# Kernel optimization log

Hardware: AMD Instinct MI355X
Metric: run time of the kernel (lower is better)

## Reference

```python
import jax, jax.numpy as jnp
import numpy as np

N = 256          # Preisach mesh resolution (n)
T = 2000         # number of applied-field time steps
H_MIN, H_MAX = 0.0, 1.0


def setup_inputs() -> dict:
    key = jax.random.key(0)
    k1, = jax.random.split(key, 1)
    h = jax.random.uniform(k1, (T,), dtype=jnp.float32)  # applied field history
    vec_shape = N * (N + 1) // 2  # = n^2/2 + n/2 = 32896
    raw_density = jnp.ones((vec_shape,), dtype=jnp.float32)  # _raw_hyst_density_vector
    offset = jnp.zeros((1,), dtype=jnp.float32)
    scale = jnp.ones((1,), dtype=jnp.float32)
    return {"h": h, "raw_density": raw_density, "offset": offset, "scale": scale}


def reference(h, raw_density, offset, scale):
    dtype = h.dtype
    # asymmetric mesh on [0,1]: alpha (yy) varies along rows, beta (xx) along cols
    x = jnp.linspace(0.0, 1.0, N, dtype=dtype)
    yy = jnp.broadcast_to(x[:, None], (N, N))  # alpha thresholds
    xx = jnp.broadcast_to(x[None, :], (N, N))  # beta thresholds
    tril_mask = jnp.tril(jnp.ones((N, N), dtype=dtype))

    h_norm = (h - H_MIN) / (H_MAX - H_MIN)  # normalize_h
    hs = jnp.concatenate([jnp.full((1,), H_MIN, dtype=dtype), h_norm])

    # initial state: all hysterions off, then tril (matches states[0] of original)
    init_state = -tril_mask

    def step(state, hp):
        h_prev, h_cur = hp
        swept_up = jnp.where(yy >= h_cur, state, 1.0)    # increasing field
        swept_down = jnp.where(xx <= h_cur, state, -1.0) # decreasing field
        new = jnp.where(h_cur > h_prev, swept_up,
                        jnp.where(h_cur < h_prev, swept_down, state))
        new = new * tril_mask  # torch.tril
        return new, new

    # scan over (hs[i-1], hs[i]) pairs -> states[1:] of the original, shape (T, N, N)
    _, states = jax.lax.scan(step, init_state, (hs[:-1], hs[1:]))

    # density: softplus then vector_to_tril (row-major lower-triangular fill)
    dens_vec = jax.nn.softplus(raw_density)
    ii, jj = jnp.tril_indices(N)
    dens = jnp.zeros((N, N), dtype=dtype).at[ii, jj].set(dens_vec)

    tri_size = N * (N + 1) / 2.0  # get_upper_trainagle_size(n)
    b = jnp.einsum('tjk,jk->t', states, dens) / tri_size
    return b * scale[0] + offset[0]
```

## Files before the change

### kernel.cpp

```cpp
#include <hip/hip_runtime.h>
#include <math.h>


#define CL 32
#define GSZ (518 * 64)
#define AS1 __attribute__((address_space(1)))
#define AS3 __attribute__((address_space(3)))

__device__ __forceinline__ int make_code(const float* __restrict__ h, int t, int T) {
    const float delta = 1.0f / 255.0f;
    int code = 256;
    if (t < T) {
        const float hc = h[t];
        const float hp = (t == 0) ? 0.0f : h[t - 1];
        if (hc > hp) {
            int i2 = (int)(hc * 255.0f);
            if (i2 > 255) i2 = 255;
            while (i2 < 255 && (float)(i2 + 1) * delta < hc) ++i2;
            while (i2 >= 0 && (float)i2 * delta >= hc) --i2;
            code = ((i2 + 1) << 16) | 256;
        } else if (hc < hp) {
            int kk = (int)(hc * 255.0f);
            if (kk > 255) kk = 255;
            while (kk < 255 && (float)(kk + 1) * delta <= hc) ++kk;
            while (kk > 0 && (float)kk * delta > hc) --kk;
            code = kk;
        }
    }
    return code;
}

__global__ __launch_bounds__(256)
void k1_compose_gbuild(const float* __restrict__ h, const float* __restrict__ raw,
                       int* __restrict__ codes, int2* __restrict__ lohi,
                       int2* __restrict__ glohi, float* __restrict__ Gg,
                       int T, int NCH, int NB1) {
    const int b = blockIdx.x;
    const int tid = threadIdx.x;
    const int w = tid >> 6, l = tid & 63;
    if (b < NB1) {
        __shared__ int2 slh[4][256];
        const int q = b * 4 + w;
        int mycode = 256;
        if (q < NCH && l < CL) {
            mycode = make_code(h, q * CL + l, T);
            codes[q * CL + l] = mycode;
        }
        int lo[4] = {-1, -1, -1, -1}, hi[4] = {256, 256, 256, 256};
        #pragma unroll
        for (int s = 0; s < CL; ++s) {
            const int cd = __shfl(mycode, s);
            const int k = cd & 0xFFFF, u = cd >> 16;
            #pragma unroll
            for (int j = 0; j < 4; ++j) {
                const int r = j * 64 + l;
                const int rr = (r < u) ? r : -1;
                lo[j] = max(min(lo[j], k), rr);
                hi[j] = max(min(hi[j], k), rr);
            }
        }
        #pragma unroll
        for (int j = 0; j < 4; ++j) {
            slh[w][j * 64 + l] = make_int2(lo[j], hi[j]);
            if (q < NCH) lohi[q * 256 + j * 64 + l] = make_int2(lo[j], hi[j]);
        }
        __syncthreads();
        int glo = -1, ghi = 256;
        #pragma unroll
        for (int w2 = 0; w2 < 4; ++w2) {
            const int2 lh = slh[w2][tid];
            glo = max(min(glo, lh.y), lh.x);
            ghi = max(min(ghi, lh.y), lh.x);
        }
        glohi[b * 256 + tid] = make_int2(glo, ghi);
    } else {
        const int r = (b - NB1) * 4 + w;
        const int tri = r * (r + 1) / 2;
        int lcol, idx0;
        if (r < 64)       { lcol = r;       idx0 = 0; }
        else if (r < 128) { lcol = r - 64;  idx0 = 259; }
        else if (r < 192) { lcol = 191 - r; idx0 = 325 + lcol; }
        else              { lcol = 255 - r; idx0 = lcol + 2; }

        float Pseg[4];
        float carry = 0.0f;
        const int nseg = r / 64 + 1;
        #pragma unroll
        for (int s = 0; s < 4; ++s) {
            Pseg[s] = 0.0f;
            if (s < nseg) {
                const int j = s * 64 + l;
                float v = 0.0f;
                if (j <= r) {
                    const float x = raw[tri + j];
                    v = fmaxf(x, 0.0f) + log1pf(expf(-fabsf(x)));
                }
                #pragma unroll
                for (int off = 1; off < 64; off <<= 1) {
                    const float t2 = __shfl_up(v, off);
                    if (l >= off) v += t2;
                }
                Pseg[s] = carry + v;
                carry += __shfl(v, 63);
            }
        }
        const float tot = carry;
        if (l == 0) Gg[idx0 * 64 + lcol] = -tot;
        #pragma unroll
        for (int s = 0; s < 4; ++s) {
            const int j = s * 64 + l;
            if (j <= r) Gg[(idx0 + 1 + j) * 64 + lcol] = 2.0f * Pseg[s] - tot;
        }
    }
}

__global__ __launch_bounds__(256)
void k3_eval(const int* __restrict__ codes, const int2* __restrict__ lohi,
             const int2* __restrict__ glohi, const float* __restrict__ Gg,
             const float* __restrict__ scale, const float* __restrict__ offset,
             float* __restrict__ out, int T, int NCH) {
    __shared__ __align__(16) float Gl[GSZ];
    __shared__ int cds[CL];
    __shared__ float cb[4 * CL];

    const int tid = threadIdx.x;
    const int w = tid >> 6, l = tid & 63;
    const int q = blockIdx.x;
    const int r = tid;

    if (tid < CL) cds[tid] = codes[q * CL + tid];

    {
        const char* gsrc = (const char*)Gg;
        char* lbase = (char*)Gl;
        #pragma unroll 8
        for (int it = 0; it < 32; ++it) {
            const int off = it * 4096 + w * 1024;
            __builtin_amdgcn_global_load_lds(
                (const AS1 void*)(gsrc + off + l * 16),
                (AS3 void*)(lbase + off), 16, 0, 0);
        }
        if (tid < 96) {
            const float4* __restrict__ Gf4 = (const float4*)Gg;
            ((float4*)Gl)[8192 + tid] = Gf4[8192 + tid];
        }
    }

    int c = -1;
    {
        const int g = q >> 2;
        #pragma unroll 8
        for (int j = 0; j < g; ++j) {
            const int2 lh = glohi[j * 256 + r];
            c = max(min(c, lh.y), lh.x);
        }
        #pragma unroll
        for (int j = g * 4; j < q; ++j) {
            const int2 lh = lohi[j * 256 + r];
            c = max(min(c, lh.y), lh.x);
        }
    }
    __syncthreads();

    int gbase, lcol;
    if (w == 0)      { gbase = 1;        lcol = l; }
    else if (w == 1) { gbase = 260;      lcol = l; }
    else if (w == 2) { gbase = 389 - l;  lcol = 63 - l; }
    else             { gbase = 66 - l;   lcol = 63 - l; }

    float myout = 0.0f;
    #pragma unroll 4
    for (int s = 0; s < CL; ++s) {
        const int cd = cds[s];
        const int k = cd & 0xFFFF, u = cd >> 16;
        c = max(min(c, k), (r < u) ? r : -1);
        float p = Gl[(gbase + c) * 64 + lcol];
        #pragma unroll
        for (int off = 32; off; off >>= 1) p += __shfl_xor(p, off);
        if (l == s) myout = p;
    }
    if (l < CL) cb[w * CL + l] = myout;
    __syncthreads();
    if (w == 0 && l < CL) {
        const int t = q * CL + l;
        if (t < T) {
            const float sum = cb[l] + cb[CL + l] + cb[2 * CL + l] + cb[3 * CL + l];
            out[t] = sum * (1.0f / 32896.0f) * scale[0] + offset[0];
        }
    }
}

extern "C" void kernel_launch(void* const* d_in, const int* in_sizes, int n_in,
                              void* d_out, int out_size, void* d_ws, size_t ws_size,
                              hipStream_t stream) {
    const float* h      = (const float*)d_in[0];
    const float* raw    = (const float*)d_in[1];
    const float* offset = (const float*)d_in[2];
    const float* scale  = (const float*)d_in[3];
    float* out = (float*)d_out;
    const int T = in_sizes[0];
    const int NCH = (T + CL - 1) / CL;
    const int NB1 = (NCH + 3) / 4;

    char* ws = (char*)d_ws;
    size_t o = 0;
    int* codes  = (int*)(ws + o);  o += ((size_t)NCH * CL * 4 + 15) & ~15ull;
    int2* lohi  = (int2*)(ws + o); o += (size_t)NCH * 256 * 8;
    int2* glohi = (int2*)(ws + o); o += (size_t)NB1 * 256 * 8;
    float* Gg   = (float*)(ws + o);

    k1_compose_gbuild<<<NB1 + 64, 256, 0, stream>>>(h, raw, codes, lohi, glohi,
                                                    Gg, T, NCH, NB1);
    k3_eval<<<NCH, 256, 0, stream>>>(codes, lohi, glohi, Gg, scale, offset,
                                     out, T, NCH);
}
```

Before: 71.32 us.

## Split eval blocks in half by row groups with atomic output accumulation

```diff
diff --git a/kernel.cpp b/kernel.cpp
--- a/kernel.cpp
+++ b/kernel.cpp
@@ -3,7 +3,8 @@
 
 
 #define CL 32
-#define GSZ (518 * 64)
+#define HROWS 259
+#define HBYTES (HROWS * 64 * 4)
 #define AS1 __attribute__((address_space(1)))
 #define AS3 __attribute__((address_space(3)))
 
@@ -34,6 +35,7 @@
 void k1_compose_gbuild(const float* __restrict__ h, const float* __restrict__ raw,
                        int* __restrict__ codes, int2* __restrict__ lohi,
                        int2* __restrict__ glohi, float* __restrict__ Gg,
+                       float* __restrict__ out, const float* __restrict__ offset,
                        int T, int NCH, int NB1) {
     const int b = blockIdx.x;
     const int tid = threadIdx.x;
@@ -74,6 +76,8 @@
         }
         glohi[b * 256 + tid] = make_int2(glo, ghi);
     } else {
+        for (int t = (b - NB1) * 256 + tid; t < T; t += 64 * 256)
+            out[t] = offset[0];
         const int r = (b - NB1) * 4 + w;
         const int tri = r * (r + 1) / 2;
         int lcol, idx0;
@@ -114,35 +118,36 @@
     }
 }
 
-__global__ __launch_bounds__(256)
+__global__ __launch_bounds__(128)
 void k3_eval(const int* __restrict__ codes, const int2* __restrict__ lohi,
              const int2* __restrict__ glohi, const float* __restrict__ Gg,
-             const float* __restrict__ scale, const float* __restrict__ offset,
-             float* __restrict__ out, int T, int NCH) {
-    __shared__ __align__(16) float Gl[GSZ];
+             const float* __restrict__ scale, float* __restrict__ out,
+             int T, int NCH) {
+    __shared__ __align__(16) float Gl[HROWS * 64];
     __shared__ int cds[CL];
-    __shared__ float cb[4 * CL];
+    __shared__ float pc[CL * 33];
 
     const int tid = threadIdx.x;
     const int w = tid >> 6, l = tid & 63;
-    const int q = blockIdx.x;
-    const int r = tid;
+    const int q = blockIdx.x >> 1;
+    const int half = blockIdx.x & 1;
+
+    const int r = half ? (w ? 128 + l : 64 + l) : (w ? 192 + l : l);
 
     if (tid < CL) cds[tid] = codes[q * CL + tid];
 
     {
-        const char* gsrc = (const char*)Gg;
+        const char* gsrc = (const char*)Gg + (size_t)half * HBYTES;
         char* lbase = (char*)Gl;
         #pragma unroll 8
         for (int it = 0; it < 32; ++it) {
-            const int off = it * 4096 + w * 1024;
+            const int off = it * 2048 + w * 1024;
             __builtin_amdgcn_global_load_lds(
                 (const AS1 void*)(gsrc + off + l * 16),
                 (AS3 void*)(lbase + off), 16, 0, 0);
         }
-        if (tid < 96) {
-            const float4* __restrict__ Gf4 = (const float4*)Gg;
-            ((float4*)Gl)[8192 + tid] = Gf4[8192 + tid];
+        if (tid < 48) {
+            ((float4*)Gl)[4096 + tid] = ((const float4*)gsrc)[4096 + tid];
         }
     }
 
@@ -163,29 +168,34 @@
     __syncthreads();
 
     int gbase, lcol;
-    if (w == 0)      { gbase = 1;        lcol = l; }
-    else if (w == 1) { gbase = 260;      lcol = l; }
-    else if (w == 2) { gbase = 389 - l;  lcol = 63 - l; }
-    else             { gbase = 66 - l;   lcol = 63 - l; }
-
-    float myout = 0.0f;
-    #pragma unroll 4
+    if (w == 0) { gbase = 1; lcol = l; }
+    else        { gbase = (half ? 130 : 66) - l; lcol = 63 - l; }
+
+    const int slot = (w << 4) | (l >> 2);
+    const bool wr = (l & 3) == 0;
+    #pragma unroll
     for (int s = 0; s < CL; ++s) {
         const int cd = cds[s];
         const int k = cd & 0xFFFF, u = cd >> 16;
         c = max(min(c, k), (r < u) ? r : -1);
         float p = Gl[(gbase + c) * 64 + lcol];
-        #pragma unroll
-        for (int off = 32; off; off >>= 1) p += __shfl_xor(p, off);
-        if (l == s) myout = p;
-    }
-    if (l < CL) cb[w * CL + l] = myout;
+        p += __shfl_xor(p, 1);
+        p += __shfl_xor(p, 2);
+        if (wr) pc[s * 33 + slot] = p;
+    }
     __syncthreads();
-    if (w == 0 && l < CL) {
-        const int t = q * CL + l;
+
+    if (tid < CL) {
+        const int t = q * CL + tid;
         if (t < T) {
-            const float sum = cb[l] + cb[CL + l] + cb[2 * CL + l] + cb[3 * CL + l];
-            out[t] = sum * (1.0f / 32896.0f) * scale[0] + offset[0];
+            const float* row = &pc[tid * 33];
+            float a0 = 0.0f, a1 = 0.0f, a2 = 0.0f, a3 = 0.0f;
+            #pragma unroll
+            for (int i = 0; i < 32; i += 4) {
+                a0 += row[i]; a1 += row[i + 1]; a2 += row[i + 2]; a3 += row[i + 3];
+            }
+            const float sum = (a0 + a1) + (a2 + a3);
+            atomicAdd(&out[t], sum * (1.0f / 32896.0f) * scale[0]);
         }
     }
 }
@@ -210,7 +220,7 @@
     float* Gg   = (float*)(ws + o);
 
     k1_compose_gbuild<<<NB1 + 64, 256, 0, stream>>>(h, raw, codes, lohi, glohi,
-                                                    Gg, T, NCH, NB1);
-    k3_eval<<<NCH, 256, 0, stream>>>(codes, lohi, glohi, Gg, scale, offset,
-                                     out, T, NCH);
-}
+                                                    Gg, out, offset, T, NCH, NB1);
+    k3_eval<<<2 * NCH, 128, 0, stream>>>(codes, lohi, glohi, Gg, scale,
+                                         out, T, NCH);
+}
```

New measurement: 71.46 us. Within noise of the previous version (+0.2%).
